# Kernel tuning notes

Hardware: AMD Instinct MI355X
Metric: run time of the kernel (lower is better)

## Reference

```python
import jax, jax.numpy as jnp
import numpy as np

B, D_IN, D_OUT = 8192, 1024, 1024


def setup_inputs() -> dict:
    key = jax.random.key(0)
    k1, k2 = jax.random.split(key)
    x = jax.random.normal(k1, (B, D_IN), dtype=jnp.float32)
    # Keras add_weight(shape=(3, input_dim, output_dim), initializer='uniform')
    kernel = jax.random.normal(k2, (3, D_IN, D_OUT), dtype=jnp.float32) * 0.05
    return {"x": x, "kernel": kernel}


def reference(x, kernel):
    # x: (B, D). Layer does expand_dims(axis=1) -> (B, 1, D) (seq_len == 1).
    output_dim = kernel.shape[-1]
    xe = x[:, None, :]                                   # (B, 1, D)
    q = jnp.einsum('bsd,do->bso', xe, kernel[0])         # (B, 1, O)
    k = jnp.einsum('bsd,do->bso', xe, kernel[1])         # (B, 1, O)
    v = jnp.einsum('bsd,do->bso', xe, kernel[2])         # (B, 1, O)
    scores = jnp.einsum('bqo,bko->bqk', q, k) / jnp.sqrt(
        jnp.asarray(output_dim, x.dtype))                # (B, 1, 1)
    attn = jax.nn.softmax(scores, axis=-1)
    out = jnp.einsum('bqk,bko->bqo', attn, v)            # (B, 1, O)
    return out
```

## Files before the change

### kernel.cpp

```cpp
#include <hip/hip_runtime.h>
#include <hip/hip_bf16.h>
#include <stdint.h>

#define AS1 __attribute__((address_space(1)))
#define AS3 __attribute__((address_space(3)))

typedef __attribute__((ext_vector_type(8))) short bf16x8_t;
typedef __attribute__((ext_vector_type(4))) float f32x4_t;

#define DDIM 1024
#define WT_ELEMS ((size_t)DDIM * DDIM)
#define XB_ELEMS ((size_t)8192 * DDIM)

static __device__ inline ushort f32_to_bf16_rne(float f) {
  union { float f; uint32_t u; } v;
  v.f = f;
  v.u += 0x7FFFu + ((v.u >> 16) & 1u);
  return (ushort)(v.u >> 16);
}

__global__ __launch_bounds__(256) void transpose_w(const float* __restrict__ W,
                                                   ushort* __restrict__ Wt) {
  __shared__ float tile[64][65];
  const int t  = threadIdx.x;
  const int bk = blockIdx.x;
  const int bn = blockIdx.y;
#pragma unroll
  for (int s = 0; s < 4; ++s) {
    const int slot = (s << 8) + t;
    const int r    = slot >> 4;
    const int c4   = (slot & 15) << 2;
    const float4 v = *(const float4*)(W + (size_t)(bk * 64 + r) * DDIM + bn * 64 + c4);
    tile[r][c4 + 0] = v.x; tile[r][c4 + 1] = v.y;
    tile[r][c4 + 2] = v.z; tile[r][c4 + 3] = v.w;
  }
  __syncthreads();
#pragma unroll
  for (int s = 0; s < 2; ++s) {
    const int slot = (s << 8) + t;
    const int n    = slot >> 3;
    const int k8   = (slot & 7) << 3;
    union { ushort h[8]; uint4 u; } tmp;
#pragma unroll
    for (int j = 0; j < 8; ++j) tmp.h[j] = f32_to_bf16_rne(tile[k8 + j][n]);
    *(uint4*)(Wt + (size_t)(bn * 64 + n) * DDIM + bk * 64 + k8) = tmp.u;
  }
}

__global__ __launch_bounds__(256) void convert_x(const float* __restrict__ X,
                                                 ushort* __restrict__ Xb) {
  const size_t i = ((size_t)blockIdx.x * 256 + threadIdx.x) << 3;
  const float4 v0 = *(const float4*)(X + i);
  const float4 v1 = *(const float4*)(X + i + 4);
  union { ushort h[8]; uint4 u; } o;
  o.h[0] = f32_to_bf16_rne(v0.x); o.h[1] = f32_to_bf16_rne(v0.y);
  o.h[2] = f32_to_bf16_rne(v0.z); o.h[3] = f32_to_bf16_rne(v0.w);
  o.h[4] = f32_to_bf16_rne(v1.x); o.h[5] = f32_to_bf16_rne(v1.y);
  o.h[6] = f32_to_bf16_rne(v1.z); o.h[7] = f32_to_bf16_rne(v1.w);
  *(uint4*)(Xb + i) = o.u;
}

__global__ __launch_bounds__(256, 2) void gemm_bb(const ushort* __restrict__ Xb,
                                                  const ushort* __restrict__ Wt,
                                                  float* __restrict__ C) {
  __shared__ __align__(16) ushort As[2][128 * 64];
  __shared__ __align__(16) ushort Bs[2][128 * 64];

  const int t    = threadIdx.x;
  const int wave = t >> 6;
  const int lane = t & 63;
  const int m0 = blockIdx.x * 128;
  const int n0 = blockIdx.y * 128;

  const int sr = t >> 3;
  const int sc = (t & 7) ^ (sr & 7);
  const ushort* aB = Xb + (size_t)(m0 + sr) * DDIM + (sc << 3);
  const ushort* bB = Wt + (size_t)(n0 + sr) * DDIM + (sc << 3);

  AS3 char* lA = (AS3 char*)&As[0][0];
  AS3 char* lB = (AS3 char*)&Bs[0][0];
  const int woff = wave << 10;

  const int wr = (wave >> 1) << 6;
  const int wc = (wave & 1) << 6;
  const int fr = lane & 15;
  const int fq = lane >> 4;

  f32x4_t acc[4][4] = {};

  auto issue = [&](int kt, int p) {
    const ushort* a = aB + kt;
    const ushort* b = bB + kt;
    AS3 char* dA = lA + (p << 14) + woff;
    AS3 char* dB = lB + (p << 14) + woff;
#pragma unroll
    for (int j = 0; j < 4; ++j) {
      __builtin_amdgcn_global_load_lds((const AS1 void*)(a + (size_t)(j << 5) * DDIM),
                                       (AS3 void*)(dA + (j << 12)), 16, 0, 0);
      __builtin_amdgcn_global_load_lds((const AS1 void*)(b + (size_t)(j << 5) * DDIM),
                                       (AS3 void*)(dB + (j << 12)), 16, 0, 0);
    }
  };

  issue(0, 0);
  __syncthreads();

  for (int i = 0; i < 16; ++i) {
    const int p = i & 1;
    if (i < 15) issue((i + 1) << 6, p ^ 1);

    const ushort* Ab = &As[p][0];
    const ushort* Bb = &Bs[p][0];
#pragma unroll
    for (int ks = 0; ks < 2; ++ks) {
      const int kc = (ks << 2) + fq;
      bf16x8_t af[4], bfr[4];
#pragma unroll
      for (int mi = 0; mi < 4; ++mi) {
        const int r = wr + (mi << 4) + fr;
        af[mi] = *(const bf16x8_t*)&Ab[(r << 6) + ((kc ^ (r & 7)) << 3)];
      }
#pragma unroll
      for (int ni = 0; ni < 4; ++ni) {
        const int r = wc + (ni << 4) + fr;
        bfr[ni] = *(const bf16x8_t*)&Bb[(r << 6) + ((kc ^ (r & 7)) << 3)];
      }
#pragma unroll
      for (int mi = 0; mi < 4; ++mi)
#pragma unroll
        for (int ni = 0; ni < 4; ++ni)
          acc[mi][ni] = __builtin_amdgcn_mfma_f32_16x16x32_bf16(af[mi], bfr[ni], acc[mi][ni], 0, 0, 0);
    }
    __syncthreads();
  }

#pragma unroll
  for (int mi = 0; mi < 4; ++mi) {
#pragma unroll
    for (int r = 0; r < 4; ++r) {
      const int row = m0 + wr + (mi << 4) + (fq << 2) + r;
      float* crow = C + (size_t)row * DDIM + n0 + wc + fr;
#pragma unroll
      for (int ni = 0; ni < 4; ++ni)
        crow[ni << 4] = acc[mi][ni][r];
    }
  }
}

__global__ __launch_bounds__(256) void gemm_xw(const float* __restrict__ X,
                                               const ushort* __restrict__ Wt,
                                               float* __restrict__ C) {
  __shared__ __align__(16) ushort As[128 * 32];
  __shared__ __align__(16) ushort Bs[128 * 32];
  const int t    = threadIdx.x;
  const int wave = t >> 6;
  const int lane = t & 63;
  const int m0 = blockIdx.x * 128;
  const int n0 = blockIdx.y * 128;
  const int srow  = (wave << 4) + (lane >> 2);
  const int skcol = (lane & 3) << 3;
  const ushort* bptr0 = Wt + (size_t)(n0 + srow) * DDIM + skcol;
  const ushort* bptr1 = Wt + (size_t)(n0 + 64 + srow) * DDIM + skcol;
  const int ar = t >> 2;
  const int ak = (t & 3) << 3;
  const float* aptr0 = X + (size_t)(m0 + ar) * DDIM + ak;
  const float* aptr1 = X + (size_t)(m0 + 64 + ar) * DDIM + ak;
  ushort* asw0 = &As[(ar << 5) + ak];
  ushort* asw1 = &As[((ar + 64) << 5) + ak];
  const int wr = (wave >> 1) << 6;
  const int wc = (wave & 1) << 6;
  const int fr = lane & 15;
  const int fq = lane >> 4;
  f32x4_t acc[4][4] = {};
  AS3 char* ldsB = (AS3 char*)Bs;
  const int woff = wave << 10;
  for (int kt = 0; kt < DDIM; kt += 32) {
    const float4 a00 = *(const float4*)(aptr0);
    const float4 a01 = *(const float4*)(aptr0 + 4);
    const float4 a10 = *(const float4*)(aptr1);
    const float4 a11 = *(const float4*)(aptr1 + 4);
    aptr0 += 32; aptr1 += 32;
    __syncthreads();
    __builtin_amdgcn_global_load_lds((const AS1 void*)bptr0, (AS3 void*)(ldsB + woff),        16, 0, 0);
    __builtin_amdgcn_global_load_lds((const AS1 void*)bptr1, (AS3 void*)(ldsB + 4096 + woff), 16, 0, 0);
    bptr0 += 32; bptr1 += 32;
    union { ushort h[8]; bf16x8_t v; } c0, c1;
    c0.h[0] = f32_to_bf16_rne(a00.x); c0.h[1] = f32_to_bf16_rne(a00.y);
    c0.h[2] = f32_to_bf16_rne(a00.z); c0.h[3] = f32_to_bf16_rne(a00.w);
    c0.h[4] = f32_to_bf16_rne(a01.x); c0.h[5] = f32_to_bf16_rne(a01.y);
    c0.h[6] = f32_to_bf16_rne(a01.z); c0.h[7] = f32_to_bf16_rne(a01.w);
    c1.h[0] = f32_to_bf16_rne(a10.x); c1.h[1] = f32_to_bf16_rne(a10.y);
    c1.h[2] = f32_to_bf16_rne(a10.z); c1.h[3] = f32_to_bf16_rne(a10.w);
    c1.h[4] = f32_to_bf16_rne(a11.x); c1.h[5] = f32_to_bf16_rne(a11.y);
    c1.h[6] = f32_to_bf16_rne(a11.z); c1.h[7] = f32_to_bf16_rne(a11.w);
    *(bf16x8_t*)asw0 = c0.v;
    *(bf16x8_t*)asw1 = c1.v;
    __syncthreads();
    bf16x8_t af[4], bfr[4];
#pragma unroll
    for (int mi = 0; mi < 4; ++mi)
      af[mi] = *(const bf16x8_t*)&As[((wr + (mi << 4) + fr) << 5) + (fq << 3)];
#pragma unroll
    for (int ni = 0; ni < 4; ++ni)
      bfr[ni] = *(const bf16x8_t*)&Bs[((wc + (ni << 4) + fr) << 5) + (fq << 3)];
#pragma unroll
    for (int mi = 0; mi < 4; ++mi)
#pragma unroll
      for (int ni = 0; ni < 4; ++ni)
        acc[mi][ni] = __builtin_amdgcn_mfma_f32_16x16x32_bf16(af[mi], bfr[ni], acc[mi][ni], 0, 0, 0);
  }
#pragma unroll
  for (int mi = 0; mi < 4; ++mi)
#pragma unroll
    for (int r = 0; r < 4; ++r) {
      const int row = m0 + wr + (mi << 4) + (fq << 2) + r;
      float* crow = C + (size_t)row * DDIM + n0 + wc + fr;
#pragma unroll
      for (int ni = 0; ni < 4; ++ni)
        crow[ni << 4] = acc[mi][ni][r];
    }
}

extern "C" void kernel_launch(void* const* d_in, const int* in_sizes, int n_in,
                              void* d_out, int out_size, void* d_ws, size_t ws_size,
                              hipStream_t stream) {
  const float* x    = (const float*)d_in[0];
  const float* kern = (const float*)d_in[1];
  const float* W = kern + (size_t)2 * DDIM * DDIM;
  ushort* Wt = (ushort*)d_ws;
  const int M = in_sizes[0] / DDIM;

  transpose_w<<<dim3(DDIM / 64, DDIM / 64), 256, 0, stream>>>(W, Wt);

  if (ws_size >= (WT_ELEMS + XB_ELEMS) * sizeof(ushort)) {
    ushort* Xb = (ushort*)d_ws + WT_ELEMS;
    convert_x<<<(unsigned)((size_t)M * DDIM / 8 / 256), 256, 0, stream>>>(x, Xb);
    gemm_bb<<<dim3(M / 128, DDIM / 128), 256, 0, stream>>>(Xb, Wt, (float*)d_out);
  } else {
    gemm_xw<<<dim3(M / 128, DDIM / 128), 256, 0, stream>>>(x, Wt, (float*)d_out);
  }
}
```

Before: 110.8 us.

## Fuse fp32-to-bf16 conversion of X into double-buffered GEMM main loop

Removes the separate convert_x pass and the bf16 copy of X in workspace. The GEMM now loads fp32 X tiles into registers one stage ahead, converts them with packed bf16 conversion instructions, and writes them to swizzled shared memory, while W tiles still stream straight into LDS. Hand-placed waitcnt and barrier instructions replace __syncthreads so the loads can overlap compute. This saves a full extra read and write of X, at the cost of more registers for prefetched A, twice the global read traffic per A tile, and fragile manual synchronisation.

```diff
diff --git a/kernel.cpp b/kernel.cpp
--- a/kernel.cpp
+++ b/kernel.cpp
@@ -10,7 +10,6 @@
 
 #define DDIM 1024
 #define WT_ELEMS ((size_t)DDIM * DDIM)
-#define XB_ELEMS ((size_t)8192 * DDIM)
 
 static __device__ inline ushort f32_to_bf16_rne(float f) {
   union { float f; uint32_t u; } v;
@@ -47,20 +46,7 @@
   }
 }
 
-__global__ __launch_bounds__(256) void convert_x(const float* __restrict__ X,
-                                                 ushort* __restrict__ Xb) {
-  const size_t i = ((size_t)blockIdx.x * 256 + threadIdx.x) << 3;
-  const float4 v0 = *(const float4*)(X + i);
-  const float4 v1 = *(const float4*)(X + i + 4);
-  union { ushort h[8]; uint4 u; } o;
-  o.h[0] = f32_to_bf16_rne(v0.x); o.h[1] = f32_to_bf16_rne(v0.y);
-  o.h[2] = f32_to_bf16_rne(v0.z); o.h[3] = f32_to_bf16_rne(v0.w);
-  o.h[4] = f32_to_bf16_rne(v1.x); o.h[5] = f32_to_bf16_rne(v1.y);
-  o.h[6] = f32_to_bf16_rne(v1.z); o.h[7] = f32_to_bf16_rne(v1.w);
-  *(uint4*)(Xb + i) = o.u;
-}
-
-__global__ __launch_bounds__(256, 2) void gemm_bb(const ushort* __restrict__ Xb,
+__global__ __launch_bounds__(256, 2) void gemm_fa(const float* __restrict__ X,
                                                   const ushort* __restrict__ Wt,
                                                   float* __restrict__ C) {
   __shared__ __align__(16) ushort As[2][128 * 64];
@@ -73,11 +59,13 @@
   const int n0 = blockIdx.y * 128;
 
   const int sr = t >> 3;
-  const int sc = (t & 7) ^ (sr & 7);
-  const ushort* aB = Xb + (size_t)(m0 + sr) * DDIM + (sc << 3);
+  const int gc = t & 7;
+  const int sc = gc ^ (sr & 7);
+  const int slotA = sc;
+
+  const float*  aB = X  + (size_t)(m0 + sr) * DDIM + (gc << 3);
   const ushort* bB = Wt + (size_t)(n0 + sr) * DDIM + (sc << 3);
 
-  AS3 char* lA = (AS3 char*)&As[0][0];
   AS3 char* lB = (AS3 char*)&Bs[0][0];
   const int woff = wave << 10;
 
@@ -88,27 +76,43 @@
 
   f32x4_t acc[4][4] = {};
 
-  auto issue = [&](int kt, int p) {
-    const ushort* a = aB + kt;
+  float4 av[8];
+
+  auto loadA = [&](int kt) {
+    const float* a = aB + kt;
+#pragma unroll
+    for (int j = 0; j < 4; ++j) {
+      av[2 * j + 0] = *(const float4*)(a + (size_t)(j << 5) * DDIM);
+      av[2 * j + 1] = *(const float4*)(a + (size_t)(j << 5) * DDIM + 4);
+    }
+  };
+
+  auto issueB = [&](int kt, int p) {
     const ushort* b = bB + kt;
-    AS3 char* dA = lA + (p << 14) + woff;
     AS3 char* dB = lB + (p << 14) + woff;
 #pragma unroll
     for (int j = 0; j < 4; ++j) {
-      __builtin_amdgcn_global_load_lds((const AS1 void*)(a + (size_t)(j << 5) * DDIM),
-                                       (AS3 void*)(dA + (j << 12)), 16, 0, 0);
       __builtin_amdgcn_global_load_lds((const AS1 void*)(b + (size_t)(j << 5) * DDIM),
                                        (AS3 void*)(dB + (j << 12)), 16, 0, 0);
     }
   };
 
-  issue(0, 0);
-  __syncthreads();
+  auto writeA = [&](int pn) {
+#pragma unroll
+    for (int j = 0; j < 4; ++j) {
+      const float4 u0 = av[2 * j + 0];
+      const float4 u1 = av[2 * j + 1];
+      uint4 w;
+      asm("v_cvt_pk_bf16_f32 %0, %1, %2" : "=v"(w.x) : "v"(u0.x), "v"(u0.y));
+      asm("v_cvt_pk_bf16_f32 %0, %1, %2" : "=v"(w.y) : "v"(u0.z), "v"(u0.w));
+      asm("v_cvt_pk_bf16_f32 %0, %1, %2" : "=v"(w.z) : "v"(u1.x), "v"(u1.y));
+      asm("v_cvt_pk_bf16_f32 %0, %1, %2" : "=v"(w.w) : "v"(u1.z), "v"(u1.w));
+      const int r = sr + (j << 5);
+      *(uint4*)&As[pn][(r << 6) + (slotA << 3)] = w;
+    }
+  };
 
-  for (int i = 0; i < 16; ++i) {
-    const int p = i & 1;
-    if (i < 15) issue((i + 1) << 6, p ^ 1);
-
+  auto compute = [&](int p) {
     const ushort* Ab = &As[p][0];
     const ushort* Bb = &Bs[p][0];
 #pragma unroll
@@ -131,7 +135,29 @@
         for (int ni = 0; ni < 4; ++ni)
           acc[mi][ni] = __builtin_amdgcn_mfma_f32_16x16x32_bf16(af[mi], bfr[ni], acc[mi][ni], 0, 0, 0);
     }
-    __syncthreads();
+  };
+
+  loadA(0);
+  issueB(0, 0);
+  writeA(0);
+  asm volatile("s_waitcnt vmcnt(0) lgkmcnt(0)\n\ts_barrier" ::: "memory");
+
+  for (int i = 0; i < 16; ++i) {
+    const int p = i & 1;
+    if (i < 15) {
+      loadA((i + 1) << 6);
+      issueB((i + 1) << 6, p ^ 1);
+      asm volatile("s_waitcnt vmcnt(12)\n\ts_barrier" ::: "memory");
+    } else {
+      asm volatile("s_waitcnt vmcnt(0)\n\ts_barrier" ::: "memory");
+    }
+
+    compute(p);
+
+    if (i < 15) {
+      writeA(p ^ 1);
+      asm volatile("s_waitcnt lgkmcnt(0)\n\ts_barrier" ::: "memory");
+    }
   }
 
 #pragma unroll
@@ -147,80 +173,6 @@
   }
 }
 
-__global__ __launch_bounds__(256) void gemm_xw(const float* __restrict__ X,
-                                               const ushort* __restrict__ Wt,
-                                               float* __restrict__ C) {
-  __shared__ __align__(16) ushort As[128 * 32];
-  __shared__ __align__(16) ushort Bs[128 * 32];
-  const int t    = threadIdx.x;
-  const int wave = t >> 6;
-  const int lane = t & 63;
-  const int m0 = blockIdx.x * 128;
-  const int n0 = blockIdx.y * 128;
-  const int srow  = (wave << 4) + (lane >> 2);
-  const int skcol = (lane & 3) << 3;
-  const ushort* bptr0 = Wt + (size_t)(n0 + srow) * DDIM + skcol;
-  const ushort* bptr1 = Wt + (size_t)(n0 + 64 + srow) * DDIM + skcol;
-  const int ar = t >> 2;
-  const int ak = (t & 3) << 3;
-  const float* aptr0 = X + (size_t)(m0 + ar) * DDIM + ak;
-  const float* aptr1 = X + (size_t)(m0 + 64 + ar) * DDIM + ak;
-  ushort* asw0 = &As[(ar << 5) + ak];
-  ushort* asw1 = &As[((ar + 64) << 5) + ak];
-  const int wr = (wave >> 1) << 6;
-  const int wc = (wave & 1) << 6;
-  const int fr = lane & 15;
-  const int fq = lane >> 4;
-  f32x4_t acc[4][4] = {};
-  AS3 char* ldsB = (AS3 char*)Bs;
-  const int woff = wave << 10;
-  for (int kt = 0; kt < DDIM; kt += 32) {
-    const float4 a00 = *(const float4*)(aptr0);
-    const float4 a01 = *(const float4*)(aptr0 + 4);
-    const float4 a10 = *(const float4*)(aptr1);
-    const float4 a11 = *(const float4*)(aptr1 + 4);
-    aptr0 += 32; aptr1 += 32;
-    __syncthreads();
-    __builtin_amdgcn_global_load_lds((const AS1 void*)bptr0, (AS3 void*)(ldsB + woff),        16, 0, 0);
-    __builtin_amdgcn_global_load_lds((const AS1 void*)bptr1, (AS3 void*)(ldsB + 4096 + woff), 16, 0, 0);
-    bptr0 += 32; bptr1 += 32;
-    union { ushort h[8]; bf16x8_t v; } c0, c1;
-    c0.h[0] = f32_to_bf16_rne(a00.x); c0.h[1] = f32_to_bf16_rne(a00.y);
-    c0.h[2] = f32_to_bf16_rne(a00.z); c0.h[3] = f32_to_bf16_rne(a00.w);
-    c0.h[4] = f32_to_bf16_rne(a01.x); c0.h[5] = f32_to_bf16_rne(a01.y);
-    c0.h[6] = f32_to_bf16_rne(a01.z); c0.h[7] = f32_to_bf16_rne(a01.w);
-    c1.h[0] = f32_to_bf16_rne(a10.x); c1.h[1] = f32_to_bf16_rne(a10.y);
-    c1.h[2] = f32_to_bf16_rne(a10.z); c1.h[3] = f32_to_bf16_rne(a10.w);
-    c1.h[4] = f32_to_bf16_rne(a11.x); c1.h[5] = f32_to_bf16_rne(a11.y);
-    c1.h[6] = f32_to_bf16_rne(a11.z); c1.h[7] = f32_to_bf16_rne(a11.w);
-    *(bf16x8_t*)asw0 = c0.v;
-    *(bf16x8_t*)asw1 = c1.v;
-    __syncthreads();
-    bf16x8_t af[4], bfr[4];
-#pragma unroll
-    for (int mi = 0; mi < 4; ++mi)
-      af[mi] = *(const bf16x8_t*)&As[((wr + (mi << 4) + fr) << 5) + (fq << 3)];
-#pragma unroll
-    for (int ni = 0; ni < 4; ++ni)
-      bfr[ni] = *(const bf16x8_t*)&Bs[((wc + (ni << 4) + fr) << 5) + (fq << 3)];
-#pragma unroll
-    for (int mi = 0; mi < 4; ++mi)
-#pragma unroll
-      for (int ni = 0; ni < 4; ++ni)
-        acc[mi][ni] = __builtin_amdgcn_mfma_f32_16x16x32_bf16(af[mi], bfr[ni], acc[mi][ni], 0, 0, 0);
-  }
-#pragma unroll
-  for (int mi = 0; mi < 4; ++mi)
-#pragma unroll
-    for (int r = 0; r < 4; ++r) {
-      const int row = m0 + wr + (mi << 4) + (fq << 2) + r;
-      float* crow = C + (size_t)row * DDIM + n0 + wc + fr;
-#pragma unroll
-      for (int ni = 0; ni < 4; ++ni)
-        crow[ni << 4] = acc[mi][ni][r];
-    }
-}
-
 extern "C" void kernel_launch(void* const* d_in, const int* in_sizes, int n_in,
                               void* d_out, int out_size, void* d_ws, size_t ws_size,
                               hipStream_t stream) {
@@ -231,12 +183,5 @@
   const int M = in_sizes[0] / DDIM;
 
   transpose_w<<<dim3(DDIM / 64, DDIM / 64), 256, 0, stream>>>(W, Wt);
-
-  if (ws_size >= (WT_ELEMS + XB_ELEMS) * sizeof(ushort)) {
-    ushort* Xb = (ushort*)d_ws + WT_ELEMS;
-    convert_x<<<(unsigned)((size_t)M * DDIM / 8 / 256), 256, 0, stream>>>(x, Xb);
-    gemm_bb<<<dim3(M / 128, DDIM / 128), 256, 0, stream>>>(Xb, Wt, (float*)d_out);
-  } else {
-    gemm_xw<<<dim3(M / 128, DDIM / 128), 256, 0, stream>>>(x, Wt, (float*)d_out);
-  }
+  gemm_fa<<<dim3(M / 128, DDIM / 128), 256, 0, stream>>>(x, Wt, (float*)d_out);
 }
```

Result: slower. 114.4 us (+3.2%).
